# Optimization experiments

Hardware: AMD Instinct MI355X
Metric: run time of the kernel (lower is better)

The kernel has to match this reference:

```python
import jax, jax.numpy as jnp
import numpy as np
from jax import lax

B, L, D = 4, 4096, 1024
H = 4
DK = D // H   # head_k_dim = 256
DV = D // H   # head_v_dim = 256
HID = max(8, D // 2)  # gate trunk hidden = 512
CHUNK = 32
CONV_K = 4
EPS = 1e-5


def silu(x):
    return x * jax.nn.sigmoid(x)


def l2norm(x):
    return x * lax.rsqrt(jnp.sum(x * x, -1, keepdims=True) + 1e-6)


def causal_dwconv_silu(x, w):
    # x: (b,l,d), w: (d,k). Depthwise causal conv1d followed by SiLU (ShortConvolution).
    k = w.shape[-1]
    xp = jnp.pad(x, ((0, 0), (k - 1, 0), (0, 0))).transpose(0, 2, 1)  # (b,d,l+k-1)
    y = lax.conv_general_dilated(xp, w[:, None, :], (1,), 'VALID',
                                 feature_group_count=w.shape[0])
    return silu(y.transpose(0, 2, 1))


def delta_rule_chunkwise(q, k, v, beta, chunk=CHUNK):
    # q,k: (b,h,l,dk), v: (b,h,l,dv), beta: (b,h,l). l assumed multiple of chunk.
    b, h, l, dk = q.shape
    dv = v.shape[-1]
    n = l // chunk
    q = l2norm(q)
    k = l2norm(k)
    v = v * beta[..., None]
    kb = k * beta[..., None]
    qc = q.reshape(b, h, n, chunk, dk)
    kc = k.reshape(b, h, n, chunk, dk)
    vc = v.reshape(b, h, n, chunk, dv)
    kbc = kb.reshape(b, h, n, chunk, dk)
    # In-chunk triangular inverse: the torch loop computes (I + tril(kb k^T, -1))^{-1}
    Lm = jnp.tril(kbc @ jnp.swapaxes(kc, -1, -2), -1)  # strictly lower
    eye = jnp.eye(chunk, dtype=q.dtype)
    Tinv = jax.scipy.linalg.solve_triangular(eye + Lm, jnp.broadcast_to(eye, Lm.shape), lower=True)
    u = Tinv @ vc   # (b,h,n,c,dv)
    w = Tinv @ kbc  # (b,h,n,c,dk)
    strict = jnp.triu(jnp.ones((chunk, chunk), bool), 1)

    def step(S, inp):
        q_i, k_i, u_i, w_i = inp  # (b,h,c,d)
        attn = jnp.where(strict, 0.0, q_i @ jnp.swapaxes(k_i, -1, -2))
        u_hat = u_i - w_i @ S
        o_i = q_i @ S + attn @ u_hat
        return S + jnp.swapaxes(k_i, -1, -2) @ u_hat, o_i

    S0 = jnp.zeros((b, h, dk, dv), q.dtype)
    xs = tuple(jnp.moveaxis(t, 2, 0) for t in (qc, kc, u, w))
    S, o = lax.scan(step, S0, xs)
    o = jnp.moveaxis(o, 0, 2).reshape(b, h, l, dv)
    return o, S


def ema_rule(v, gamma):
    # v: (b,h,l,d), gamma: (b,h,l). Causal EMA: s_t = g_t*s_{t-1} + (1-g_t)*v_t
    def step(state, inp):
        v_t, g_t = inp
        state = g_t[..., None] * state + (1.0 - g_t[..., None]) * v_t
        return state, state

    s0 = jnp.zeros((v.shape[0], v.shape[1], v.shape[3]), v.dtype)
    _, out = lax.scan(step, s0, (jnp.moveaxis(v, 2, 0), jnp.moveaxis(gamma, 2, 0)))
    return jnp.moveaxis(out, 0, 2)


def hierarchical_gate(x, Wtrunk, btrunk, Wcoarse, bcoarse, Wlocal, blocal, Wglobal, bglobal, log_temp_c, log_temp_f):
    b, l, _ = x.shape
    z = silu(x @ Wtrunk.T + btrunk)  # (b,l,HID)
    tc = (jax.nn.softplus(log_temp_c) + 1e-4)[None, None, :, None]  # (1,1,h,1)
    tf = (jax.nn.softplus(log_temp_f) + 1e-4)[None, None, :, None]
    pg = jax.nn.softmax((z @ Wcoarse.T + bcoarse).reshape(b, l, H, 2) / tc, axis=-1)
    q = jax.nn.softmax((z @ Wlocal.T + blocal).reshape(b, l, H, 2) / tf, axis=-1)
    r = jax.nn.softmax((z @ Wglobal.T + bglobal).reshape(b, l, H, 2) / tf, axis=-1)
    w_v = pg[..., 0:1] * q[..., 0:1]
    w_es = pg[..., 0:1] * q[..., 1:2]
    w_d = pg[..., 1:2] * r[..., 0:1]
    w_el = pg[..., 1:2] * r[..., 1:2]
    return jnp.concatenate([w_v, w_es, w_d, w_el], axis=-1)  # (b,l,h,4)


def setup_inputs() -> dict:
    key = jax.random.key(0)
    ks = jax.random.split(key, 20)
    s = 0.02
    inp = {
        'hidden_states': jax.random.normal(ks[0], (B, L, D), jnp.float32),
        'Wq': jax.random.normal(ks[1], (D, D), jnp.float32) * s,
        'Wk': jax.random.normal(ks[2], (D, D), jnp.float32) * s,
        'Wv': jax.random.normal(ks[3], (D, D), jnp.float32) * s,
        'conv_q_w': jax.random.normal(ks[4], (D, CONV_K), jnp.float32) * 0.5,
        'conv_k_w': jax.random.normal(ks[5], (D, CONV_K), jnp.float32) * 0.5,
        'conv_v_w': jax.random.normal(ks[6], (D, CONV_K), jnp.float32) * 0.5,
        'Wb': jax.random.normal(ks[7], (H, D), jnp.float32) * s,
        'Wds': jax.random.normal(ks[8], (H, D), jnp.float32) * s,
        'bds': jnp.full((H,), -2.9444, jnp.float32),
        'Wdl': jax.random.normal(ks[9], (H, D), jnp.float32) * s,
        'bdl': jnp.full((H,), 2.9444, jnp.float32),
        'Wtrunk': jax.random.normal(ks[10], (HID, D), jnp.float32) * s,
        'btrunk': jnp.zeros((HID,), jnp.float32),
        'Wcoarse': jax.random.normal(ks[11], (H * 2, HID), jnp.float32) * s,
        'bcoarse': jnp.ones((H * 2,), jnp.float32),
        'Wlocal': jax.random.normal(ks[12], (H * 2, HID), jnp.float32) * s,
        'blocal': jnp.zeros((H * 2,), jnp.float32).at[::2].set(1.0),
        'Wglobal': jax.random.normal(ks[13], (H * 2, HID), jnp.float32) * s,
        'bglobal': jnp.zeros((H * 2,), jnp.float32).at[::2].set(1.0),
        'log_temp_c': jnp.zeros((H,), jnp.float32),  # log(1.0)
        'log_temp_f': jnp.zeros((H,), jnp.float32),
        'o_norm_w': jnp.ones((DV,), jnp.float32),
        'Wo': jax.random.normal(ks[14], (D, D), jnp.float32) * s,
    }
    return inp


def reference(hidden_states, Wq, Wk, Wv, conv_q_w, conv_k_w, conv_v_w, Wb, Wds, bds, Wdl, bdl,
              Wtrunk, btrunk, Wcoarse, bcoarse, Wlocal, blocal, Wglobal, bglobal,
              log_temp_c, log_temp_f, o_norm_w, Wo):
    x = hidden_states
    b, l, _ = x.shape
    # projections + short causal depthwise conv + SiLU
    q = causal_dwconv_silu(x @ Wq.T, conv_q_w).reshape(b, l, H, DK).transpose(0, 2, 1, 3)
    k = causal_dwconv_silu(x @ Wk.T, conv_k_w).reshape(b, l, H, DK).transpose(0, 2, 1, 3)
    v = causal_dwconv_silu(x @ Wv.T, conv_v_w).reshape(b, l, H, DV).transpose(0, 2, 1, 3)
    beta = jax.nn.sigmoid(x @ Wb.T).transpose(0, 2, 1)  # (b,h,l)
    delta_o, _ = delta_rule_chunkwise(q, k, v, beta)
    g_s = jax.nn.sigmoid(x @ Wds.T + bds).transpose(0, 2, 1)  # (b,h,l) short decay
    g_l = jax.nn.sigmoid(x @ Wdl.T + bdl).transpose(0, 2, 1)  # long decay
    ema_s = ema_rule(v, g_s)
    ema_l = ema_rule(v, g_l)
    weights = hierarchical_gate(x, Wtrunk, btrunk, Wcoarse, bcoarse, Wlocal, blocal,
                                Wglobal, bglobal, log_temp_c, log_temp_f)  # (b,l,h,4) [V,Es,D,El]
    v_b = v.transpose(0, 2, 1, 3)
    o = (weights[..., 0:1] * v_b
         + weights[..., 1:2] * ema_s.transpose(0, 2, 1, 3)
         + weights[..., 2:3] * delta_o.transpose(0, 2, 1, 3)
         + weights[..., 3:4] * ema_l.transpose(0, 2, 1, 3))
    # per-head RMSNorm
    o = o * lax.rsqrt(jnp.mean(o * o, -1, keepdims=True) + EPS) * o_norm_w
    return o.reshape(b, l, D) @ Wo.T
```

## Files before the change

kernel.cpp:

```cpp
#include <hip/hip_runtime.h>
#include <math.h>

#define BB 4
#define LL 4096
#define DD 1024
#define HH 4
#define DKk 256
#define DVv 256
#define HIDD 512
#define NC 128
#define NSEG 64
#define SEG 64

typedef unsigned short ushort_t;
typedef __attribute__((ext_vector_type(8))) short short8;
typedef __attribute__((ext_vector_type(4))) float floatx4;

__device__ __forceinline__ float sigm(float x) { return 1.f / (1.f + __expf(-x)); }

__device__ __forceinline__ float bf2f(ushort_t u) {
  union { unsigned int i; float f; } c; c.i = ((unsigned int)u) << 16; return c.f;
}
__device__ __forceinline__ ushort_t f2bf(float f) {
  union { float f; unsigned int i; } c; c.f = f;
  unsigned int lsb = (c.i >> 16) & 1u;
  return (ushort_t)((c.i + 0x7fffu + lsb) >> 16);
}
__device__ __forceinline__ void unpack2(unsigned int u, float& a, float& b) {
  union { unsigned int i; float f; } c0, c1;
  c0.i = u << 16; c1.i = u & 0xffff0000u; a = c0.f; b = c1.f;
}
__device__ __forceinline__ unsigned int pack2(float a, float b) {
  return (unsigned int)f2bf(a) | ((unsigned int)f2bf(b) << 16);
}
__device__ __forceinline__ void unpack8(const uint4 v, float* o) {
  unpack2(v.x, o[0], o[1]); unpack2(v.y, o[2], o[3]);
  unpack2(v.z, o[4], o[5]); unpack2(v.w, o[6], o[7]);
}
__device__ __forceinline__ float ubits(unsigned u) {
  union { unsigned i; float f; } c; c.i = u; return c.f;
}
__device__ __forceinline__ void split2t(float a, float b, unsigned& hi, unsigned& lo) {
  union { float f; unsigned u; } ca, cb; ca.f = a; cb.f = b;
  const unsigned ha = ca.u & 0xffff0000u, hb = cb.u & 0xffff0000u;
  hi = (ha >> 16) | hb;
  union { float f; unsigned u; } la, lb;
  la.f = a - ubits(ha); lb.f = b - ubits(hb);
  lo = (la.u >> 16) | (lb.u & 0xffff0000u);
}
__device__ __forceinline__ void gload16(const ushort_t* g, ushort_t* l) {
  __builtin_amdgcn_global_load_lds(
      (const __attribute__((address_space(1))) void*)g,
      (__attribute__((address_space(3))) void*)l, 16, 0, 0);
}

__global__ __launch_bounds__(256) void cvt_all_kernel(
    const float* __restrict__ x,  const float* __restrict__ Wq,
    const float* __restrict__ Wk, const float* __restrict__ Wv,
    const float* __restrict__ Wo, const float* __restrict__ Wtr,
    ushort_t* __restrict__ xb,  ushort_t* __restrict__ Wqb,
    ushort_t* __restrict__ Wkb, ushort_t* __restrict__ Wvb,
    ushort_t* __restrict__ Wob, ushort_t* __restrict__ Wtrb)
{
  const int NX = (int)((size_t)BB*LL*DD/8), NW = DD*DD/8, NT = HIDD*DD/8;
  int i = blockIdx.x * 256 + threadIdx.x;
  const float* src; ushort_t* dst;
  if (i < NX) { src = x; dst = xb; }
  else {
    i -= NX;
    if (i < NW) { src = Wq; dst = Wqb; }
    else { i -= NW;
      if (i < NW) { src = Wk; dst = Wkb; }
      else { i -= NW;
        if (i < NW) { src = Wv; dst = Wvb; }
        else { i -= NW;
          if (i < NW) { src = Wo; dst = Wob; }
          else { i -= NW; if (i >= NT) return; src = Wtr; dst = Wtrb; }
        }
      }
    }
  }
  const float4 a = ((const float4*)src)[2*i];
  const float4 b = ((const float4*)src)[2*i + 1];
  uint4 p;
  p.x = pack2(a.x, a.y); p.y = pack2(a.z, a.w);
  p.z = pack2(b.x, b.y); p.w = pack2(b.z, b.w);
  ((uint4*)dst)[i] = p;
}

template<int ACT, int BF16OUT>
__global__ __launch_bounds__(256) void gemm_bf16(const ushort_t* __restrict__ A,
    const ushort_t* __restrict__ W, const float* __restrict__ bias,
    void* __restrict__ Cv, int M, int N, int K)
{
  __shared__ ushort_t As[128*32];
  __shared__ ushort_t Ws[128*32];
  const int tid = threadIdx.x;
  const int bm = blockIdx.y * 128, bn = blockIdx.x * 128;
  const int lane = tid & 63, wave = tid >> 6;
  const int wm = (wave >> 1) * 64, wn = (wave & 1) * 64;
  const int fr = lane & 15, fq = lane >> 4;
  const int srow = wave * 16 + (lane >> 2);
  const int scol = (lane & 3) * 8;
  const ushort_t* Ap = A + (size_t)(bm + srow) * K + scol;
  const ushort_t* Wp = W + (size_t)(bn + srow) * K + scol;
  ushort_t* AsD = &As[wave * 512];
  ushort_t* WsD = &Ws[wave * 512];
  floatx4 acc[4][4];
#pragma unroll
  for (int i = 0; i < 4; ++i)
#pragma unroll
    for (int j = 0; j < 4; ++j) acc[i][j] = (floatx4){0.f, 0.f, 0.f, 0.f};

  for (int k0 = 0; k0 < K; k0 += 32) {
    __syncthreads();
    gload16(Ap + k0, AsD);
    gload16(Ap + (size_t)64 * K + k0, AsD + 64*32);
    gload16(Wp + k0, WsD);
    gload16(Wp + (size_t)64 * K + k0, WsD + 64*32);
    __syncthreads();
    short8 af[4], bf_[4];
#pragma unroll
    for (int mt = 0; mt < 4; ++mt)
      af[mt] = *(const short8*)&As[(wm + mt*16 + fr)*32 + fq*8];
#pragma unroll
    for (int nt = 0; nt < 4; ++nt)
      bf_[nt] = *(const short8*)&Ws[(wn + nt*16 + fr)*32 + fq*8];
#pragma unroll
    for (int mt = 0; mt < 4; ++mt)
#pragma unroll
      for (int nt = 0; nt < 4; ++nt)
        acc[mt][nt] = __builtin_amdgcn_mfma_f32_16x16x32_bf16(af[mt], bf_[nt], acc[mt][nt], 0, 0, 0);
  }
#pragma unroll
  for (int mt = 0; mt < 4; ++mt) {
#pragma unroll
    for (int reg = 0; reg < 4; ++reg) {
      const int row = bm + wm + mt*16 + fq*4 + reg;
#pragma unroll
      for (int nt = 0; nt < 4; ++nt) {
        const int col = bn + wn + nt*16 + fr;
        float v = acc[mt][nt][reg];
        if (ACT == 1) { v += bias[col]; v = v * sigm(v); }
        if (BF16OUT) ((ushort_t*)Cv)[(size_t)row * N + col] = f2bf(v);
        else         ((float*)Cv)[(size_t)row * N + col] = v;
      }
    }
  }
}

__global__ __launch_bounds__(256) void conv_silu_kernel(const ushort_t* __restrict__ xin,
    const float* __restrict__ wc, ushort_t* __restrict__ outp)
{
  const size_t i8 = (size_t)blockIdx.x * 256 + threadIdx.x;
  const int d8 = (int)((i8 & 127) << 3);
  const int l  = (int)((i8 >> 7) & (LL - 1));
  const int b  = (int)(i8 >> 19);
  const ushort_t* xp = xin + i8 * 8;
  const uint4 z4 = (uint4){0u,0u,0u,0u};
  const uint4 v0 = *(const uint4*)xp;
  const uint4 v1 = (l >= 1) ? *(const uint4*)(xp - DD)   : z4;
  const uint4 v2 = (l >= 2) ? *(const uint4*)(xp - 2*DD) : z4;
  const uint4 v3 = (l >= 3) ? *(const uint4*)(xp - 3*DD) : z4;
  float x0[8], x1[8], x2[8], x3[8];
  unpack8(v0, x0); unpack8(v1, x1); unpack8(v2, x2); unpack8(v3, x3);
  unsigned pk[4];
#pragma unroll
  for (int p = 0; p < 4; ++p) {
    float o2[2];
#pragma unroll
    for (int q = 0; q < 2; ++q) {
      const int j = p*2 + q;
      const float4 w = *(const float4*)(wc + (d8 + j) * 4);
      float acc = w.w * x0[j];
      acc = fmaf(w.z, x1[j], acc);
      acc = fmaf(w.y, x2[j], acc);
      acc = fmaf(w.x, x3[j], acc);
      o2[q] = acc * sigm(acc);
    }
    pk[p] = pack2(o2[0], o2[1]);
  }
  const int h = d8 >> 8, dk = d8 & 255;
  *(uint4*)(outp + (((size_t)(b*HH + h))*LL + l)*DKk + dk) = *(uint4*)pk;
}

__global__ __launch_bounds__(256) void small_proj_kernel(const float* __restrict__ x,
   const float* __restrict__ Wb, const float* __restrict__ Wds, const float* __restrict__ bds,
   const float* __restrict__ Wdl, const float* __restrict__ bdl,
   float* __restrict__ beta, float* __restrict__ gs, float* __restrict__ gl)
{
  const int bl = blockIdx.x;
  const int t = threadIdx.x, wave = t >> 6, lane = t & 63;
  __shared__ float res[12];
  const float* xr = x + (size_t)bl * DD + lane * 16;
  const float4 x0 = *(const float4*)(xr);
  const float4 x1 = *(const float4*)(xr + 4);
  const float4 x2 = *(const float4*)(xr + 8);
  const float4 x3 = *(const float4*)(xr + 12);
  for (int rr = 0; rr < 3; ++rr) {
    const int r = wave * 3 + rr;
    const int mat = r >> 2, h = r & 3;
    const float* Wr = (mat == 0 ? Wb : (mat == 1 ? Wds : Wdl)) + (size_t)h * DD + lane * 16;
    const float4 w0 = *(const float4*)(Wr);
    const float4 w1 = *(const float4*)(Wr + 4);
    const float4 w2 = *(const float4*)(Wr + 8);
    const float4 w3 = *(const float4*)(Wr + 12);
    float p = x0.x*w0.x + x0.y*w0.y + x0.z*w0.z + x0.w*w0.w
            + x1.x*w1.x + x1.y*w1.y + x1.z*w1.z + x1.w*w1.w
            + x2.x*w2.x + x2.y*w2.y + x2.z*w2.z + x2.w*w2.w
            + x3.x*w3.x + x3.y*w3.y + x3.z*w3.z + x3.w*w3.w;
#pragma unroll
    for (int o = 1; o < 64; o <<= 1) p += __shfl_xor(p, o);
    if (lane == 0) res[r] = p;
  }
  __syncthreads();
  if (t < 12) {
    const int mat = t >> 2, h = t & 3;
    float v = res[t];
    if (mat == 1) v += bds[h];
    if (mat == 2) v += bdl[h];
    v = sigm(v);
    const int b = bl >> 12, l = bl & (LL - 1);
    const size_t o = ((size_t)(b*HH + h))*LL + l;
    (mat == 0 ? beta : (mat == 1 ? gs : gl))[o] = v;
  }
}

__global__ __launch_bounds__(256) void gate_kernel(const ushort_t* __restrict__ z,
  const float* __restrict__ Wc, const float* __restrict__ bc,
  const float* __restrict__ Wl, const float* __restrict__ bl_,
  const float* __restrict__ Wg, const float* __restrict__ bg,
  const float* __restrict__ ltc, const float* __restrict__ ltf,
  float* __restrict__ wgt)
{
  const int bl = blockIdx.x;
  const int t = threadIdx.x, wave = t >> 6, lane = t & 63;
  __shared__ float res[24];
  const uint4 zv = *(const uint4*)(z + (size_t)bl * HIDD + lane * 8);
  float zf[8]; unpack8(zv, zf);
  for (int rr = 0; rr < 6; ++rr) {
    const int r = wave * 6 + rr;
    const int mat = r >> 3, qi = r & 7;
    const float* Wr = (mat == 0 ? Wc : (mat == 1 ? Wl : Wg)) + (size_t)qi * HIDD + lane * 8;
    const float4 w0 = *(const float4*)(Wr);
    const float4 w1 = *(const float4*)(Wr + 4);
    float p = zf[0]*w0.x + zf[1]*w0.y + zf[2]*w0.z + zf[3]*w0.w
            + zf[4]*w1.x + zf[5]*w1.y + zf[6]*w1.z + zf[7]*w1.w;
#pragma unroll
    for (int o = 1; o < 64; o <<= 1) p += __shfl_xor(p, o);
    if (lane == 0) {
      const float* br = (mat == 0 ? bc : (mat == 1 ? bl_ : bg));
      res[r] = p + br[qi];
    }
  }
  __syncthreads();
  if (t < 4) {
    const float tc = logf(1.f + __expf(ltc[t])) + 1e-4f;
    const float tf = logf(1.f + __expf(ltf[t])) + 1e-4f;
    const float pg0 = sigm((res[2*t]     - res[2*t+1])     / tc);
    const float q0  = sigm((res[8+2*t]   - res[8+2*t+1])   / tf);
    const float r0  = sigm((res[16+2*t]  - res[16+2*t+1])  / tf);
    float* o = wgt + ((size_t)bl * HH + t) * 4;
    o[0] = pg0 * q0;         o[1] = pg0 * (1.f - q0);
    o[2] = (1.f - pg0) * r0; o[3] = (1.f - pg0) * (1.f - r0);
  }
}

#define QS 264
__global__ __launch_bounds__(256) void prep_kernel(ushort_t* __restrict__ q,
    ushort_t* __restrict__ k, const ushort_t* __restrict__ v,
    const float* __restrict__ beta,
    ushort_t* __restrict__ u, ushort_t* __restrict__ w,
    ushort_t* __restrict__ ah, ushort_t* __restrict__ al)
{
  __shared__ ushort_t qb[32*QS];
  __shared__ ushort_t kb[32*QS];
  __shared__ float Lm[32*32];
  __shared__ float betas[32];
  const int bid = blockIdx.x;
  const int ci = bid & (NC - 1);
  const int bh = bid >> 7;
  const int t = threadIdx.x;
  const size_t base = ((size_t)bh * LL + ci*32) * DKk;
  if (t < 32) betas[t] = beta[(size_t)bh * LL + ci*32 + t];
  for (int i4 = t; i4 < 1024; i4 += 256) {
    const int r = i4 >> 5, e = (i4 & 31) * 8;
    *(uint4*)&qb[r*QS + e] = *(const uint4*)(q + base + r*256 + e);
    *(uint4*)&kb[r*QS + e] = *(const uint4*)(k + base + r*256 + e);
  }
  __syncthreads();
  {
    const int r = t >> 3, g = t & 7;
    const int e0 = g * 32;
    float qf[32], kf[32];
#pragma unroll
    for (int j = 0; j < 4; ++j) {
      const uint4 qv = *(const uint4*)&qb[r*QS + e0 + j*8];
      const uint4 kv = *(const uint4*)&kb[r*QS + e0 + j*8];
      unpack8(qv, qf + j*8); unpack8(kv, kf + j*8);
    }
    float sq = 0.f, sk = 0.f;
#pragma unroll
    for (int j = 0; j < 32; ++j) {
      sq = fmaf(qf[j], qf[j], sq);
      sk = fmaf(kf[j], kf[j], sk);
    }
#pragma unroll
    for (int o = 1; o < 8; o <<= 1) { sq += __shfl_xor(sq, o); sk += __shfl_xor(sk, o); }
    const float rq = rsqrtf(sq + 1e-6f), rk = rsqrtf(sk + 1e-6f);
#pragma unroll
    for (int j = 0; j < 4; ++j) {
      uint4 qo, ko;
      qo.x = pack2(qf[j*8+0]*rq, qf[j*8+1]*rq);
      qo.y = pack2(qf[j*8+2]*rq, qf[j*8+3]*rq);
      qo.z = pack2(qf[j*8+4]*rq, qf[j*8+5]*rq);
      qo.w = pack2(qf[j*8+6]*rq, qf[j*8+7]*rq);
      ko.x = pack2(kf[j*8+0]*rk, kf[j*8+1]*rk);
      ko.y = pack2(kf[j*8+2]*rk, kf[j*8+3]*rk);
      ko.z = pack2(kf[j*8+4]*rk, kf[j*8+5]*rk);
      ko.w = pack2(kf[j*8+6]*rk, kf[j*8+7]*rk);
      *(uint4*)&qb[r*QS + e0 + j*8] = qo;
      *(uint4*)&kb[r*QS + e0 + j*8] = ko;
    }
  }
  __syncthreads();
  for (int i4 = t; i4 < 1024; i4 += 256) {
    const int r = i4 >> 5, e = (i4 & 31) * 8;
    *(uint4*)(q + base + r*256 + e) = *(const uint4*)&qb[r*QS + e];
  }
  {
    unsigned int pk[16];
#pragma unroll
    for (int j = 0; j < 16; ++j)
      pk[j] = (unsigned int)kb[(2*j)*QS + t] | ((unsigned int)kb[(2*j+1)*QS + t] << 16);
    uint4* kd = (uint4*)(k + base + (size_t)t*32);
#pragma unroll
    for (int j = 0; j < 4; ++j) kd[j] = ((const uint4*)pk)[j];
  }
  {
    const int lane = t & 63, wv4 = t >> 6;
    const int fr = lane & 15, fq = lane >> 4;
    const int it = wv4 >> 1, jt = wv4 & 1;
    floatx4 dq = (floatx4){0.f,0.f,0.f,0.f};
    floatx4 dk2 = (floatx4){0.f,0.f,0.f,0.f};
#pragma unroll
    for (int ks = 0; ks < 8; ++ks) {
      const short8 bfk = *(const short8*)&kb[(jt*16+fr)*QS + ks*32 + fq*8];
      const short8 afq = *(const short8*)&qb[(it*16+fr)*QS + ks*32 + fq*8];
      const short8 afk = *(const short8*)&kb[(it*16+fr)*QS + ks*32 + fq*8];
      dq  = __builtin_amdgcn_mfma_f32_16x16x32_bf16(afq, bfk, dq, 0,0,0);
      dk2 = __builtin_amdgcn_mfma_f32_16x16x32_bf16(afk, bfk, dk2, 0,0,0);
    }
#pragma unroll
    for (int reg = 0; reg < 4; ++reg) {
      const int i = it*16 + fq*4 + reg;
      const int j = jt*16 + fr;
      const float av = (j <= i) ? dq[reg] : 0.f;
      const ushort_t hh = f2bf(av);
      const size_t aoff = ((size_t)bh*NC + ci)*1024 + (size_t)i*32 + j;
      ah[aoff] = hh;
      al[aoff] = f2bf(av - bf2f(hh));
      Lm[i*32 + j] = (j < i) ? betas[i] * dk2[reg] : 0.f;
    }
  }
  __syncthreads();
  {
    float cu[32], cw[32];
#pragma unroll
    for (int r = 0; r < 32; ++r) {
      cu[r] = bf2f(v[base + r*256 + t]) * betas[r];
      cw[r] = bf2f(kb[r*QS + t]) * betas[r];
    }
#pragma unroll
    for (int i = 1; i < 32; ++i) {
      float au = cu[i], aw = cw[i];
#pragma unroll
      for (int j = 0; j < i; ++j) {
        const float lm = Lm[i*32 + j];
        au = fmaf(-lm, cu[j], au);
        aw = fmaf(-lm, cw[j], aw);
      }
      cu[i] = au; cw[i] = aw;
    }
    {
      unsigned int pu[16];
#pragma unroll
      for (int j = 0; j < 16; ++j) pu[j] = pack2(cu[2*j], cu[2*j+1]);
      uint4* ud = (uint4*)(u + base + (size_t)t*32);
#pragma unroll
      for (int j = 0; j < 4; ++j) ud[j] = ((const uint4*)pu)[j];
    }
#pragma unroll
    for (int r = 0; r < 32; ++r) w[base + r*256 + t] = f2bf(cw[r]);
  }
}

#define S16(dv,kk) (((dv)<<8) + ((kk) ^ (((dv)&7)<<3)))
#define U16(dv,cr) (((dv)<<5) + ((cr) ^ (((dv)&3)<<3)))

struct FragsK { short8 kf[4]; short8 afh, afl; };
struct FragsA { short8 aw[8]; uint2 uu; };

__global__ __launch_bounds__(256, 1) void scan_kernel(
    const ushort_t* __restrict__ qn, const ushort_t* __restrict__ kt,
    const ushort_t* __restrict__ ut, const ushort_t* __restrict__ w,
    const ushort_t* __restrict__ ah, const ushort_t* __restrict__ al,
    float* __restrict__ dout)
{
  __shared__ ushort_t STh[16*256];
  __shared__ ushort_t STl[16*256];
  __shared__ ushort_t Uh[16*32];
  __shared__ ushort_t Ul[16*32];
  const int bid = blockIdx.x;
  const int bh = bid & 15, vs = bid >> 4;
  const int b = bh >> 2, h = bh & 3;
  const int t = threadIdx.x, lane = t & 63, wv = t >> 6;
  const int fr = lane & 15, fq = lane >> 4;
  const int mt = wv & 1;
  const bool isW = (wv < 2);

  for (int i = t; i < 512; i += 256) {
    ((uint4*)STh)[i] = (uint4){0u,0u,0u,0u};
    ((uint4*)STl)[i] = (uint4){0u,0u,0u,0u};
  }

  const size_t bhL = (size_t)bh * LL;
  const ushort_t* wqB = (isW ? w : qn) + bhL * DKk;
  const ushort_t* kB  = kt + bhL * DKk;
  const ushort_t* uB  = ut + bhL * DVv;
  const ushort_t* ahB = ah + (size_t)bh * NC * 1024;
  const ushort_t* alB = al + (size_t)bh * NC * 1024;
  float* oB = dout + (size_t)b * LL * DD + h * DVv + vs * 16 + fr;

  floatx4 Sacc[4];
#pragma unroll
  for (int i = 0; i < 4; ++i) Sacc[i] = (floatx4){0.f,0.f,0.f,0.f};

  auto loadK = [&](int ci, FragsK& f) {
    const ushort_t* kp = kB + (size_t)ci*8192 + (size_t)(wv*64 + fr)*32 + fq*8;
#pragma unroll
    for (int m = 0; m < 4; ++m) f.kf[m] = *(const short8*)(kp + m*512);
    if (!isW) {
      f.afh = *(const short8*)(ahB + (size_t)ci*1024 + (mt*16+fr)*32 + fq*8);
      f.afl = *(const short8*)(alB + (size_t)ci*1024 + (mt*16+fr)*32 + fq*8);
    }
  };
  auto loadA = [&](int ci, FragsA& f) {
    const ushort_t* ap = wqB + (size_t)(ci*32 + mt*16 + fr) * DKk + fq*8;
#pragma unroll
    for (int ks = 0; ks < 8; ++ks) f.aw[ks] = *(const short8*)(ap + ks*32);
    if (isW)
      f.uu = *(const uint2*)(uB + (size_t)ci*8192 + (size_t)(vs*16 + fr)*32 + mt*16 + fq*4);
  };

  FragsK k0, k1; FragsA a0, a1;
  loadK(0, k0);
  loadA(0, a0);
  __syncthreads();

  auto body = [&](int ci, FragsK& kc, FragsK& kn, FragsA& ac, FragsA& an) {
    if (ci + 1 < NC) { loadK(ci + 1, kn); loadA(ci + 1, an); }
    floatx4 acc0, acc1;
    if (isW) {
      float u0,u1,u2,u3; unpack2(ac.uu.x,u0,u1); unpack2(ac.uu.y,u2,u3);
      acc0 = (floatx4){-u0,-u1,-u2,-u3};
      acc1 = (floatx4){0.f,0.f,0.f,0.f};
#pragma unroll
      for (int ks = 0; ks < 8; ++ks) {
        const short8 sh = *(const short8*)&STh[S16(fr, ks*32 + fq*8)];
        const short8 sl = *(const short8*)&STl[S16(fr, ks*32 + fq*8)];
        acc0 = __builtin_amdgcn_mfma_f32_16x16x32_bf16(ac.aw[ks], sh, acc0, 0,0,0);
        acc1 = __builtin_amdgcn_mfma_f32_16x16x32_bf16(ac.aw[ks], sl, acc1, 0,0,0);
      }
      const float v0 = -(acc0[0]+acc1[0]), v1 = -(acc0[1]+acc1[1]);
      const float v2 = -(acc0[2]+acc1[2]), v3 = -(acc0[3]+acc1[3]);
      unsigned ph0, pl0, ph1, pl1;
      split2t(v0, v1, ph0, pl0); split2t(v2, v3, ph1, pl1);
      *(uint2*)&Uh[U16(fr, mt*16 + fq*4)] = (uint2){ph0, ph1};
      *(uint2*)&Ul[U16(fr, mt*16 + fq*4)] = (uint2){pl0, pl1};
    } else {
      acc0 = (floatx4){0.f,0.f,0.f,0.f};
#pragma unroll
      for (int ks = 0; ks < 8; ++ks) {
        const short8 sh = *(const short8*)&STh[S16(fr, ks*32 + fq*8)];
        acc0 = __builtin_amdgcn_mfma_f32_16x16x32_bf16(ac.aw[ks], sh, acc0, 0,0,0);
      }
    }
    __syncthreads();
    const short8 uhh = *(const short8*)&Uh[U16(fr, fq*8)];
    const short8 uhl = *(const short8*)&Ul[U16(fr, fq*8)];
    if (!isW) {
      acc0 = __builtin_amdgcn_mfma_f32_16x16x32_bf16(kc.afh, uhh, acc0, 0,0,0);
      acc0 = __builtin_amdgcn_mfma_f32_16x16x32_bf16(kc.afh, uhl, acc0, 0,0,0);
      acc0 = __builtin_amdgcn_mfma_f32_16x16x32_bf16(kc.afl, uhh, acc0, 0,0,0);
      float* op = oB + (size_t)(ci*32 + mt*16 + fq*4) * DD;
#pragma unroll
      for (int r = 0; r < 4; ++r) op[(size_t)r * DD] = acc0[r];
    }
#pragma unroll
    for (int m = 0; m < 4; ++m) {
      Sacc[m] = __builtin_amdgcn_mfma_f32_16x16x32_bf16(kc.kf[m], uhh, Sacc[m], 0,0,0);
      Sacc[m] = __builtin_amdgcn_mfma_f32_16x16x32_bf16(kc.kf[m], uhl, Sacc[m], 0,0,0);
    }
#pragma unroll
    for (int m = 0; m < 4; ++m) {
      unsigned ph0, pl0, ph1, pl1;
      split2t(Sacc[m][0], Sacc[m][1], ph0, pl0);
      split2t(Sacc[m][2], Sacc[m][3], ph1, pl1);
      const int dk0 = wv*64 + m*16 + fq*4;
      *(uint2*)&STh[S16(fr, dk0)] = (uint2){ph0, ph1};
      *(uint2*)&STl[S16(fr, dk0)] = (uint2){pl0, pl1};
    }
    __syncthreads();
  };

  for (int c2 = 0; c2 < NC; c2 += 2) {
    body(c2,     k0, k1, a0, a1);
    body(c2 + 1, k1, k0, a1, a0);
  }
}

__global__ __launch_bounds__(256) void ema_local_kernel(const ushort_t* __restrict__ v,
  const float* __restrict__ gs, const float* __restrict__ gl,
  ushort_t* __restrict__ es, ushort_t* __restrict__ el,
  float* __restrict__ Bs, float* __restrict__ Bl,
  float* __restrict__ As, float* __restrict__ Al,
  float* __restrict__ PfS, float* __restrict__ PfL)
{
  const int bid = blockIdx.x;
  const int seg = bid & (NSEG - 1), bh = bid >> 6;
  const int b = bh >> 2, h = bh & 3;
  const int dv = threadIdx.x;
  const int l0 = seg * SEG;
  const ushort_t* vp = v + ((size_t)bh*LL + l0) * DVv + dv;
  const float* gsp = gs + (size_t)bh*LL + l0;
  const float* glp = gl + (size_t)bh*LL + l0;
  ushort_t* esp = es + ((size_t)b*LL + l0)*DD + h*DVv + dv;
  ushort_t* elp = el + ((size_t)b*LL + l0)*DD + h*DVv + dv;
  float* pfs = PfS + (size_t)bh*LL + l0;
  float* pfl = PfL + (size_t)bh*LL + l0;
  float s1 = 0.f, s2 = 0.f, p1 = 1.f, p2 = 1.f;
  for (int j = 0; j < SEG; ++j) {
    const float vv = bf2f(vp[(size_t)j * DVv]);
    const float a = gsp[j], g2 = glp[j];
    s1 = fmaf(a,  s1, (1.f - a)  * vv);
    s2 = fmaf(g2, s2, (1.f - g2) * vv);
    p1 *= a; p2 *= g2;
    esp[(size_t)j * DD] = f2bf(s1);
    elp[(size_t)j * DD] = f2bf(s2);
    if (dv == 0) { pfs[j] = p1; pfl[j] = p2; }
  }
  const size_t o = (((size_t)bh*NSEG + seg) << 8) + dv;
  Bs[o] = s1; Bl[o] = s2;
  if (dv == 0) { As[bh*NSEG + seg] = p1; Al[bh*NSEG + seg] = p2; }
}

__global__ __launch_bounds__(256) void ema_carry_kernel(
  const float* __restrict__ Bs, const float* __restrict__ Bl,
  const float* __restrict__ As, const float* __restrict__ Al,
  float* __restrict__ Cs, float* __restrict__ Cl)
{
  const int bh = blockIdx.x;
  const int dv = threadIdx.x;
  __shared__ float Ash[NSEG], Alh[NSEG];
  if (dv < NSEG) { Ash[dv] = As[bh*NSEG + dv]; Alh[dv] = Al[bh*NSEG + dv]; }
  __syncthreads();
  float c1 = 0.f, c2 = 0.f;
  for (int s = 0; s < NSEG; ++s) {
    const size_t o = (((size_t)bh*NSEG + s) << 8) + dv;
    Cs[o] = c1; Cl[o] = c2;
    c1 = fmaf(Ash[s], c1, Bs[o]);
    c2 = fmaf(Alh[s], c2, Bl[o]);
  }
}

__global__ __launch_bounds__(64) void combine_kernel(const ushort_t* __restrict__ v,
  const ushort_t* __restrict__ es, const ushort_t* __restrict__ el,
  const float* __restrict__ dov, const float* __restrict__ wgt,
  const float* __restrict__ onw,
  const float* __restrict__ Cs, const float* __restrict__ Cl,
  const float* __restrict__ PfS, const float* __restrict__ PfL,
  ushort_t* __restrict__ outp)
{
  const int bid = blockIdx.x;
  const int h = bid & 3;
  const size_t bl = (size_t)(bid >> 2);
  const int lane = threadIdx.x;
  const size_t b = bl >> 12;
  const size_t l = bl & (LL - 1);
  const int bh = (int)(b * HH) + h;
  const int seg = (int)(l >> 6);
  const size_t vidx = (((b*HH + h) * (size_t)LL) + l) * DVv + lane*4;
  const size_t didx = bl * DD + h*DVv + lane*4;
  const uint2 vu = *(const uint2*)(v + vidx);
  const uint2 eu = *(const uint2*)(es + didx);
  const uint2 gu = *(const uint2*)(el + didx);
  const float4 d4 = *(const float4*)(dov + didx);
  const float pS = PfS[(size_t)bh*LL + l];
  const float pL = PfL[(size_t)bh*LL + l];
  const float4 cs4 = *(const float4*)(Cs + (((size_t)bh*NSEG + seg) << 8) + lane*4);
  const float4 cl4 = *(const float4*)(Cl + (((size_t)bh*NSEG + seg) << 8) + lane*4);
  float vf[4], ef[4], gf[4];
  unpack2(vu.x, vf[0], vf[1]); unpack2(vu.y, vf[2], vf[3]);
  unpack2(eu.x, ef[0], ef[1]); unpack2(eu.y, ef[2], ef[3]);
  unpack2(gu.x, gf[0], gf[1]); unpack2(gu.y, gf[2], gf[3]);
  ef[0] = fmaf(pS, cs4.x, ef[0]); ef[1] = fmaf(pS, cs4.y, ef[1]);
  ef[2] = fmaf(pS, cs4.z, ef[2]); ef[3] = fmaf(pS, cs4.w, ef[3]);
  gf[0] = fmaf(pL, cl4.x, gf[0]); gf[1] = fmaf(pL, cl4.y, gf[1]);
  gf[2] = fmaf(pL, cl4.z, gf[2]); gf[3] = fmaf(pL, cl4.w, gf[3]);
  const float* wp = wgt + (size_t)bid * 4;
  const float w0 = wp[0], w1 = wp[1], w2 = wp[2], w3 = wp[3];
  float o[4];
  const float df[4] = {d4.x, d4.y, d4.z, d4.w};
  float ss = 0.f;
#pragma unroll
  for (int i = 0; i < 4; ++i) {
    o[i] = w0*vf[i] + w1*ef[i] + w2*df[i] + w3*gf[i];
    ss = fmaf(o[i], o[i], ss);
  }
#pragma unroll
  for (int off = 1; off < 64; off <<= 1) ss += __shfl_xor(ss, off);
  const float sc = rsqrtf(ss * (1.f / DVv) + 1e-5f);
  const float4 nw = *(const float4*)(onw + lane*4);
  uint2 pk;
  pk.x = pack2(o[0]*sc*nw.x, o[1]*sc*nw.y);
  pk.y = pack2(o[2]*sc*nw.z, o[3]*sc*nw.w);
  *(uint2*)(outp + didx) = pk;
}

extern "C" void kernel_launch(void* const* d_in, const int* in_sizes, int n_in,
                              void* d_out, int out_size, void* d_ws, size_t ws_size,
                              hipStream_t stream)
{
  const float* x    = (const float*)d_in[0];
  const float* Wq   = (const float*)d_in[1];
  const float* Wk   = (const float*)d_in[2];
  const float* Wv   = (const float*)d_in[3];
  const float* cqw  = (const float*)d_in[4];
  const float* ckw  = (const float*)d_in[5];
  const float* cvw  = (const float*)d_in[6];
  const float* Wb   = (const float*)d_in[7];
  const float* Wds  = (const float*)d_in[8];
  const float* bds  = (const float*)d_in[9];
  const float* Wdl  = (const float*)d_in[10];
  const float* bdl  = (const float*)d_in[11];
  const float* Wtr  = (const float*)d_in[12];
  const float* btr  = (const float*)d_in[13];
  const float* Wc   = (const float*)d_in[14];
  const float* bc   = (const float*)d_in[15];
  const float* Wl   = (const float*)d_in[16];
  const float* blc  = (const float*)d_in[17];
  const float* Wg   = (const float*)d_in[18];
  const float* bg   = (const float*)d_in[19];
  const float* ltc  = (const float*)d_in[20];
  const float* ltf  = (const float*)d_in[21];
  const float* onw  = (const float*)d_in[22];
  const float* Wo   = (const float*)d_in[23];
  float* outp = (float*)d_out;

  const size_t BLD = (size_t)BB * LL * DD;
  unsigned char* w8 = (unsigned char*)d_ws;
  const size_t SL = BLD * 2;
  ushort_t* SA = (ushort_t*)(w8 + 0*SL);
  ushort_t* SB = (ushort_t*)(w8 + 1*SL);
  ushort_t* SC = (ushort_t*)(w8 + 2*SL);
  ushort_t* SD = (ushort_t*)(w8 + 3*SL);
  ushort_t* SE = (ushort_t*)(w8 + 4*SL);
  ushort_t* zb   = (ushort_t*)(w8 + 5*SL);
  ushort_t* attn_hi = (ushort_t*)(w8 + 5*SL + BLD);
  ushort_t* attn_lo = attn_hi + (size_t)BB*HH*NC*1024;
  float*    beta = (float*)(attn_hi + 2*(size_t)BB*HH*NC*1024);
  float*    gs   = beta + (size_t)BB*HH*LL;
  float*    gl   = gs   + (size_t)BB*HH*LL;
  float*    wgt  = gl   + (size_t)BB*HH*LL;
  float*    Bs   = wgt  + (size_t)BB*LL*HH*4;
  float*    Bl   = Bs   + (size_t)BB*HH*NSEG*256;
  float*    Cs   = Bl   + (size_t)BB*HH*NSEG*256;
  float*    Cl   = Cs   + (size_t)BB*HH*NSEG*256;
  float*    As   = Cl   + (size_t)BB*HH*NSEG*256;
  float*    Al   = As   + (size_t)BB*HH*NSEG;
  float*    PfS  = Al   + (size_t)BB*HH*NSEG;
  float*    PfL  = PfS  + (size_t)BB*HH*LL;
  ushort_t* Wqb  = (ushort_t*)(PfL + (size_t)BB*HH*LL);
  ushort_t* Wkb  = Wqb + (size_t)DD*DD;
  ushort_t* Wvb  = Wkb + (size_t)DD*DD;
  ushort_t* Wob  = Wvb + (size_t)DD*DD;
  ushort_t* Wtrb = Wob + (size_t)DD*DD;
  ushort_t* xb   = SD;
  float*    dov  = outp;

  const int MBL = BB * LL;
  dim3 blk256(256);

  {
    const int NTOT = (int)(BLD/8) + 4*(DD*DD/8) + HIDD*DD/8;
    cvt_all_kernel<<<dim3((NTOT + 255)/256), blk256, 0, stream>>>(
        x, Wq, Wk, Wv, Wo, Wtr, xb, Wqb, Wkb, Wvb, Wob, Wtrb);
  }

  gemm_bf16<0,1><<<dim3(DD/128, MBL/128), blk256, 0, stream>>>(xb, Wqb, nullptr, SA, MBL, DD, DD);
  gemm_bf16<0,1><<<dim3(DD/128, MBL/128), blk256, 0, stream>>>(xb, Wkb, nullptr, SB, MBL, DD, DD);
  gemm_bf16<0,1><<<dim3(DD/128, MBL/128), blk256, 0, stream>>>(xb, Wvb, nullptr, SC, MBL, DD, DD);
  gemm_bf16<1,1><<<dim3(HIDD/128, MBL/128), blk256, 0, stream>>>(xb, Wtrb, btr, zb, MBL, HIDD, DD);
  small_proj_kernel<<<dim3(MBL), blk256, 0, stream>>>(x, Wb, Wds, bds, Wdl, bdl, beta, gs, gl);
  gate_kernel<<<dim3(MBL), blk256, 0, stream>>>(zb, Wc, bc, Wl, blc, Wg, bg, ltc, ltf, wgt);
  conv_silu_kernel<<<dim3((unsigned)(BLD/8/256)), blk256, 0, stream>>>(SA, cqw, SD);
  conv_silu_kernel<<<dim3((unsigned)(BLD/8/256)), blk256, 0, stream>>>(SB, ckw, SA);
  conv_silu_kernel<<<dim3((unsigned)(BLD/8/256)), blk256, 0, stream>>>(SC, cvw, SB);
  prep_kernel<<<dim3(BB*HH*NC), blk256, 0, stream>>>(SD, SA, SB, beta, SC, SE, attn_hi, attn_lo);
  scan_kernel<<<dim3(256), blk256, 0, stream>>>(SD, SA, SC, SE, attn_hi, attn_lo, dov);
  ema_local_kernel<<<dim3(BB*HH*NSEG), blk256, 0, stream>>>(SB, gs, gl, SE, SD, Bs, Bl, As, Al, PfS, PfL);
  ema_carry_kernel<<<dim3(BB*HH), blk256, 0, stream>>>(Bs, Bl, As, Al, Cs, Cl);
  combine_kernel<<<dim3(MBL*HH), dim3(64), 0, stream>>>(SB, SE, SD, dov, wgt, onw, Cs, Cl, PfS, PfL, SA);
  gemm_bf16<0,0><<<dim3(DD/128, MBL/128), blk256, 0, stream>>>(SA, Wob, nullptr, outp, MBL, DD, DD);
}
```

Before: 1.034 ms.

## Fuse Q/K/V/trunk projections into one GEMM, pack combine blocks, vectorize Lm reads

Reorders the bf16 weight buffers so Wq, Wk, Wv and Wtrunk sit contiguously, then replaces four projection GEMM launches with a single launch over a 3584-wide concatenated output. The epilogue routes each 128-column tile to the right destination and applies bias plus SiLU only for trunk tiles. This cuts launch overhead and tail effects, and lets every tile of the x operand be shared across all four projections. Separately, the combine kernel now packs four 64-thread rows into each 256-thread block, and the triangular solve in the prep kernel reads Lm as float4.

New measurement: 1.016 ms. About the same (-1.7%).

```diff
diff --git a/kernel.cpp b/kernel.cpp
--- a/kernel.cpp
+++ b/kernel.cpp
@@ -57,10 +57,10 @@
 __global__ __launch_bounds__(256) void cvt_all_kernel(
     const float* __restrict__ x,  const float* __restrict__ Wq,
     const float* __restrict__ Wk, const float* __restrict__ Wv,
-    const float* __restrict__ Wo, const float* __restrict__ Wtr,
+    const float* __restrict__ Wtr, const float* __restrict__ Wo,
     ushort_t* __restrict__ xb,  ushort_t* __restrict__ Wqb,
     ushort_t* __restrict__ Wkb, ushort_t* __restrict__ Wvb,
-    ushort_t* __restrict__ Wob, ushort_t* __restrict__ Wtrb)
+    ushort_t* __restrict__ Wtrb, ushort_t* __restrict__ Wob)
 {
   const int NX = (int)((size_t)BB*LL*DD/8), NW = DD*DD/8, NT = HIDD*DD/8;
   int i = blockIdx.x * 256 + threadIdx.x;
@@ -74,8 +74,8 @@
       else { i -= NW;
         if (i < NW) { src = Wv; dst = Wvb; }
         else { i -= NW;
-          if (i < NW) { src = Wo; dst = Wob; }
-          else { i -= NW; if (i >= NT) return; src = Wtr; dst = Wtrb; }
+          if (i < NT) { src = Wtr; dst = Wtrb; }
+          else { i -= NT; if (i >= NW) return; src = Wo; dst = Wob; }
         }
       }
     }
@@ -144,6 +144,76 @@
         if (ACT == 1) { v += bias[col]; v = v * sigm(v); }
         if (BF16OUT) ((ushort_t*)Cv)[(size_t)row * N + col] = f2bf(v);
         else         ((float*)Cv)[(size_t)row * N + col] = v;
+      }
+    }
+  }
+}
+
+__global__ __launch_bounds__(256) void gemm_qkvt(const ushort_t* __restrict__ A,
+    const ushort_t* __restrict__ Wcat, const float* __restrict__ btr,
+    ushort_t* __restrict__ Cq, ushort_t* __restrict__ Ck,
+    ushort_t* __restrict__ Cvv, ushort_t* __restrict__ Cz, int M, int K)
+{
+  __shared__ ushort_t As[128*32];
+  __shared__ ushort_t Ws[128*32];
+  const int tid = threadIdx.x;
+  const int bm = blockIdx.y * 128, bn = blockIdx.x * 128;
+  const int lane = tid & 63, wave = tid >> 6;
+  const int wm = (wave >> 1) * 64, wn = (wave & 1) * 64;
+  const int fr = lane & 15, fq = lane >> 4;
+  const int srow = wave * 16 + (lane >> 2);
+  const int scol = (lane & 3) * 8;
+  const ushort_t* Ap = A + (size_t)(bm + srow) * K + scol;
+  const ushort_t* Wp = Wcat + (size_t)(bn + srow) * K + scol;
+  ushort_t* AsD = &As[wave * 512];
+  ushort_t* WsD = &Ws[wave * 512];
+  floatx4 acc[4][4];
+#pragma unroll
+  for (int i = 0; i < 4; ++i)
+#pragma unroll
+    for (int j = 0; j < 4; ++j) acc[i][j] = (floatx4){0.f, 0.f, 0.f, 0.f};
+
+  for (int k0 = 0; k0 < K; k0 += 32) {
+    __syncthreads();
+    gload16(Ap + k0, AsD);
+    gload16(Ap + (size_t)64 * K + k0, AsD + 64*32);
+    gload16(Wp + k0, WsD);
+    gload16(Wp + (size_t)64 * K + k0, WsD + 64*32);
+    __syncthreads();
+    short8 af[4], bf_[4];
+#pragma unroll
+    for (int mt = 0; mt < 4; ++mt)
+      af[mt] = *(const short8*)&As[(wm + mt*16 + fr)*32 + fq*8];
+#pragma unroll
+    for (int nt = 0; nt < 4; ++nt)
+      bf_[nt] = *(const short8*)&Ws[(wn + nt*16 + fr)*32 + fq*8];
+#pragma unroll
+    for (int mt = 0; mt < 4; ++mt)
+#pragma unroll
+      for (int nt = 0; nt < 4; ++nt)
+        acc[mt][nt] = __builtin_amdgcn_mfma_f32_16x16x32_bf16(af[mt], bf_[nt], acc[mt][nt], 0, 0, 0);
+  }
+  const bool trunk = (bn >= 3072);
+  ushort_t* dst;
+  int nloc, cbase;
+  if (!trunk) {
+    const int mat = bn >> 10;
+    dst = (mat == 0 ? Cq : (mat == 1 ? Ck : Cvv));
+    nloc = 1024; cbase = bn & 1023;
+  } else {
+    dst = Cz; nloc = 512; cbase = bn - 3072;
+  }
+#pragma unroll
+  for (int mt = 0; mt < 4; ++mt) {
+#pragma unroll
+    for (int reg = 0; reg < 4; ++reg) {
+      const int row = bm + wm + mt*16 + fq*4 + reg;
+#pragma unroll
+      for (int nt = 0; nt < 4; ++nt) {
+        const int col = cbase + wn + nt*16 + fr;
+        float v = acc[mt][nt][reg];
+        if (trunk) { v += btr[col]; v = v * sigm(v); }
+        dst[(size_t)row * nloc + col] = f2bf(v);
       }
     }
   }
@@ -375,10 +445,17 @@
     for (int i = 1; i < 32; ++i) {
       float au = cu[i], aw = cw[i];
 #pragma unroll
-      for (int j = 0; j < i; ++j) {
-        const float lm = Lm[i*32 + j];
-        au = fmaf(-lm, cu[j], au);
-        aw = fmaf(-lm, cw[j], aw);
+      for (int jb = 0; jb < (i + 3) / 4; ++jb) {
+        const float4 lr = *(const float4*)&Lm[i*32 + jb*4];
+        const float lmv[4] = {lr.x, lr.y, lr.z, lr.w};
+#pragma unroll
+        for (int qv = 0; qv < 4; ++qv) {
+          const int j = jb*4 + qv;
+          if (j < i) {
+            au = fmaf(-lmv[qv], cu[j], au);
+            aw = fmaf(-lmv[qv], cw[j], aw);
+          }
+        }
       }
       cu[i] = au; cw[i] = aw;
     }
@@ -574,7 +651,7 @@
   }
 }
 
-__global__ __launch_bounds__(64) void combine_kernel(const ushort_t* __restrict__ v,
+__global__ __launch_bounds__(256) void combine_kernel(const ushort_t* __restrict__ v,
   const ushort_t* __restrict__ es, const ushort_t* __restrict__ el,
   const float* __restrict__ dov, const float* __restrict__ wgt,
   const float* __restrict__ onw,
@@ -582,10 +659,10 @@
   const float* __restrict__ PfS, const float* __restrict__ PfL,
   ushort_t* __restrict__ outp)
 {
-  const int bid = blockIdx.x;
+  const int bid = blockIdx.x * 4 + (threadIdx.x >> 6);
   const int h = bid & 3;
   const size_t bl = (size_t)(bid >> 2);
-  const int lane = threadIdx.x;
+  const int lane = threadIdx.x & 63;
   const size_t b = bl >> 12;
   const size_t l = bl & (LL - 1);
   const int bh = (int)(b * HH) + h;
@@ -684,8 +761,8 @@
   ushort_t* Wqb  = (ushort_t*)(PfL + (size_t)BB*HH*LL);
   ushort_t* Wkb  = Wqb + (size_t)DD*DD;
   ushort_t* Wvb  = Wkb + (size_t)DD*DD;
-  ushort_t* Wob  = Wvb + (size_t)DD*DD;
-  ushort_t* Wtrb = Wob + (size_t)DD*DD;
+  ushort_t* Wtrb = Wvb + (size_t)DD*DD;
+  ushort_t* Wob  = Wtrb + (size_t)HIDD*DD;
   ushort_t* xb   = SD;
   float*    dov  = outp;
 
@@ -695,13 +772,10 @@
   {
     const int NTOT = (int)(BLD/8) + 4*(DD*DD/8) + HIDD*DD/8;
     cvt_all_kernel<<<dim3((NTOT + 255)/256), blk256, 0, stream>>>(
-        x, Wq, Wk, Wv, Wo, Wtr, xb, Wqb, Wkb, Wvb, Wob, Wtrb);
-  }
-
-  gemm_bf16<0,1><<<dim3(DD/128, MBL/128), blk256, 0, stream>>>(xb, Wqb, nullptr, SA, MBL, DD, DD);
-  gemm_bf16<0,1><<<dim3(DD/128, MBL/128), blk256, 0, stream>>>(xb, Wkb, nullptr, SB, MBL, DD, DD);
-  gemm_bf16<0,1><<<dim3(DD/128, MBL/128), blk256, 0, stream>>>(xb, Wvb, nullptr, SC, MBL, DD, DD);
-  gemm_bf16<1,1><<<dim3(HIDD/128, MBL/128), blk256, 0, stream>>>(xb, Wtrb, btr, zb, MBL, HIDD, DD);
+        x, Wq, Wk, Wv, Wtr, Wo, xb, Wqb, Wkb, Wvb, Wtrb, Wob);
+  }
+
+  gemm_qkvt<<<dim3(28, MBL/128), blk256, 0, stream>>>(xb, Wqb, btr, SA, SB, SC, zb, MBL, DD);
   small_proj_kernel<<<dim3(MBL), blk256, 0, stream>>>(x, Wb, Wds, bds, Wdl, bdl, beta, gs, gl);
   gate_kernel<<<dim3(MBL), blk256, 0, stream>>>(zb, Wc, bc, Wl, blc, Wg, bg, ltc, ltf, wgt);
   conv_silu_kernel<<<dim3((unsigned)(BLD/8/256)), blk256, 0, stream>>>(SA, cqw, SD);
@@ -711,6 +785,6 @@
   scan_kernel<<<dim3(256), blk256, 0, stream>>>(SD, SA, SC, SE, attn_hi, attn_lo, dov);
   ema_local_kernel<<<dim3(BB*HH*NSEG), blk256, 0, stream>>>(SB, gs, gl, SE, SD, Bs, Bl, As, Al, PfS, PfL);
   ema_carry_kernel<<<dim3(BB*HH), blk256, 0, stream>>>(Bs, Bl, As, Al, Cs, Cl);
-  combine_kernel<<<dim3(MBL*HH), dim3(64), 0, stream>>>(SB, SE, SD, dov, wgt, onw, Cs, Cl, PfS, PfL, SA);
+  combine_kernel<<<dim3(MBL*HH/4), blk256, 0, stream>>>(SB, SE, SD, dov, wgt, onw, Cs, Cl, PfS, PfL, SA);
   gemm_bf16<0,0><<<dim3(DD/128, MBL/128), blk256, 0, stream>>>(SA, Wob, nullptr, outp, MBL, DD, DD);
 }
```
